# Optimization experiments

Hardware: AMD Instinct MI355X
Metric: run time of the kernel (lower is better)

Reference implementation:

```python
import jax, jax.numpy as jnp
import numpy as np

B, N, DIM_IN, DIM_INNER, DIM_OUT, WINDOW = 4, 4096, 1024, 1024, 1024, 128


def setup_inputs() -> dict:
    key = jax.random.key(0)
    k1, k2, k3, k4 = jax.random.split(key, 4)
    x = jax.random.normal(k1, (B, N, DIM_IN), dtype=jnp.float32)
    # to_qkv: Linear(dim_in, 3*dim_inner, bias=False); stored as [in, 3*inner] for x @ W
    w_qkv = jax.random.normal(k2, (DIM_IN, 3 * DIM_INNER), dtype=jnp.float32) / np.sqrt(DIM_IN)
    # to_out: Linear(dim_inner, dim_out) with bias
    w_out = jax.random.normal(k3, (DIM_INNER, DIM_OUT), dtype=jnp.float32) / np.sqrt(DIM_INNER)
    b_out = jax.random.normal(k4, (DIM_OUT,), dtype=jnp.float32) * 0.01
    return {"x": x, "w_qkv": w_qkv, "w_out": w_out, "b_out": b_out}


def reference(x, w_qkv, w_out, b_out):
    b, n, _ = x.shape
    w = WINDOW
    scale = DIM_INNER ** (-0.5)
    # n is a multiple of window, so pad_to_multiple is a no-op
    qkv = jnp.einsum('bnd,de->bne', x, w_qkv)
    q, k, v = jnp.split(qkv, 3, axis=-1)
    nw = n // w
    win = lambda t: t.reshape(b, nw, w, DIM_INNER)  # b (w n) d -> b w n d
    q, k, v = win(q), win(k), win(v)
    # pad one zero block at the front of the window axis
    kp = jnp.pad(k, ((0, 0), (1, 0), (0, 0), (0, 0)))
    # concat previous block + current block along token axis -> (b, nw, 2w, d)
    k2 = jnp.concatenate([kp[:, :-1], kp[:, 1:]], axis=2)
    # NOTE: faithful to source bug: the lambda references k (not t), so v is
    # overwritten with the concatenated k blocks as well.
    v2 = k2
    sim = jnp.einsum('bwid,bwjd->bwij', q, k2) * scale  # (b, nw, w, 2w)
    i, j = w, 2 * w
    mask = jnp.triu(jnp.ones((i, j), dtype=bool), j - i + 1)  # causal within lookback window
    mask_value = -jnp.finfo(sim.dtype).max
    sim = jnp.where(mask[None, None], mask_value, sim)
    attn = jax.nn.softmax(sim, axis=-1)
    out = jnp.einsum('bwij,bwjd->bwid', attn, v2)
    out = out.reshape(b, n, DIM_INNER)[:, :n]
    return jnp.einsum('bnd,de->bne', out, w_out) + b_out
```

## Files before the change

### kernel.cpp

```cpp
#include <hip/hip_runtime.h>
#include <float.h>


#define B_SZ 4
#define SEQ 4096
#define DIM 1024
#define WIN 128
#define NWIN 32
#define TW 256
#define NROWS (B_SZ * SEQ)
#define KPAD 4224

typedef float f32x4 __attribute__((ext_vector_type(4)));
typedef __bf16 bf16x8 __attribute__((ext_vector_type(8)));

__device__ __forceinline__ unsigned short f2b(float f) {
    unsigned int u = __float_as_uint(f);
    u += 0x7FFF + ((u >> 16) & 1);
    return (unsigned short)(u >> 16);
}

__device__ __forceinline__ void gld_lds16(const unsigned short* g, unsigned short* l) {
    __builtin_amdgcn_global_load_lds(
        (const __attribute__((address_space(1))) void*)g,
        (__attribute__((address_space(3))) void*)l, 16, 0, 0);
}

__device__ __forceinline__ bf16x8 lds_read_swz(const unsigned short* tb, int row, int kbyte) {
    int L = row * 128 + kbyte;
    L ^= ((L >> 9) & 1) << 5;
    return *(const bf16x8*)((const char*)tb + L);
}

#define BAR __builtin_amdgcn_s_barrier()
#define PRI1 __builtin_amdgcn_s_setprio(1)
#define PRI0 __builtin_amdgcn_s_setprio(0)
#define WAIT_LGKM0 do { asm volatile("s_waitcnt lgkmcnt(0)" ::: "memory"); \
                        __builtin_amdgcn_sched_barrier(0); } while (0)
#define WAIT_VM8   do { asm volatile("s_waitcnt vmcnt(8)" ::: "memory");  \
                        __builtin_amdgcn_sched_barrier(0); } while (0)
#define WAIT_VM0   do { asm volatile("s_waitcnt vmcnt(0)" ::: "memory");  \
                        __builtin_amdgcn_sched_barrier(0); } while (0)

#define LDAF(BUF, MH)                                                        \
    _Pragma("unroll") for (int m_ = 0; m_ < 4; ++m_)                         \
    _Pragma("unroll") for (int ks_ = 0; ks_ < 2; ++ks_)                      \
        afq[MH][m_][ks_] = lds_read_swz(bufA[BUF],                           \
            wr * 128 + (MH) * 64 + m_ * 16 + fr, ks_ * 64 + kby);

#define LDBF(BUF, NH)                                                        \
    _Pragma("unroll") for (int n_ = 0; n_ < 2; ++n_)                         \
    _Pragma("unroll") for (int ks_ = 0; ks_ < 2; ++ks_)                      \
        bfq[n_][ks_] = lds_read_swz(bufB[BUF],                               \
            wc * 64 + (NH) * 32 + n_ * 16 + fr, ks_ * 64 + kby);

#define MFQ(MH, NH)                                                          \
    _Pragma("unroll") for (int ks_ = 0; ks_ < 2; ++ks_)                      \
    _Pragma("unroll") for (int m_ = 0; m_ < 4; ++m_)                         \
    _Pragma("unroll") for (int n_ = 0; n_ < 2; ++n_)                         \
        acc[(MH) * 4 + m_][(NH) * 2 + n_] =                                  \
            __builtin_amdgcn_mfma_f32_16x16x32_bf16(afq[MH][m_][ks_],        \
                bfq[n_][ks_], acc[(MH) * 4 + m_][(NH) * 2 + n_], 0, 0, 0);

#define STG_A(BUF, HJ, K0) gld_lds16(A + soffA[HJ] + (K0), bufA[BUF] + ldst[HJ])
#define STG_B(BUF, HJ, K0) gld_lds16(Bt + soffB[HJ] + (K0), bufB[BUF] + ldst[HJ])

#define PHASES03(BUF, KST, ST)                                               \
    LDAF(BUF, 0); LDBF(BUF, 0);                                              \
    BAR; WAIT_LGKM0; PRI1; MFQ(0, 0); PRI0; BAR;                             \
    LDAF(BUF, 1);                                                            \
    BAR; WAIT_LGKM0; PRI1; MFQ(1, 0); PRI0; BAR;                             \
    LDBF(BUF, 1);                                                            \
    if (ST) { STG_A(BUF, 0, KST); STG_A(BUF, 1, KST);                        \
              STG_A(BUF, 2, KST); STG_A(BUF, 3, KST); }                      \
    BAR; WAIT_LGKM0; PRI1; MFQ(1, 1); PRI0; BAR;                             \
    if (ST) { STG_B(BUF, 0, KST); STG_B(BUF, 1, KST);                        \
              STG_B(BUF, 2, KST); STG_B(BUF, 3, KST); }                      \
    BAR; WAIT_LGKM0; PRI1; MFQ(0, 1); PRI0;

__device__ __forceinline__ void core256(
    const unsigned short* __restrict__ A, int lda,
    const unsigned short* __restrict__ Bt, int ldb, int K,
    unsigned short* lds, f32x4 (&acc)[8][4],
    int wid, int lane, int wr, int wc)
{
    unsigned short* bufA[2] = { lds, lds + 32768 };
    unsigned short* bufB[2] = { lds + 16384, lds + 49152 };

    const int kby = (lane >> 4) * 16;
    const int fr = lane & 15;

    int soffA[4], soffB[4], ldst[4];
#pragma unroll
    for (int hj = 0; hj < 4; ++hj) {
        const int half = hj >> 1, j = hj & 1;
        const int P = half * 16384 + wid * 2048 + j * 1024 + lane * 16;
        const int L = P ^ (((P >> 9) & 1) << 5);
        const int row = L >> 7, col = (L & 127) >> 1;
        soffA[hj] = row * lda + col;
        soffB[hj] = row * ldb + col;
        ldst[hj] = (half * 16384 + wid * 2048 + j * 1024) >> 1;
    }

    bf16x8 afq[2][4][2], bfq[2][2];
#pragma unroll
    for (int m = 0; m < 8; ++m)
#pragma unroll
        for (int n = 0; n < 4; ++n) acc[m][n] = (f32x4){0.f, 0.f, 0.f, 0.f};

#pragma unroll
    for (int hj = 0; hj < 4; ++hj) STG_A(0, hj, 0);
#pragma unroll
    for (int hj = 0; hj < 4; ++hj) STG_B(0, hj, 0);
#pragma unroll
    for (int hj = 0; hj < 4; ++hj) STG_A(1, hj, 64);
#pragma unroll
    for (int hj = 0; hj < 4; ++hj) STG_B(1, hj, 64);
    WAIT_VM8;
    BAR;

    const int NITER = K >> 7;
#pragma unroll 1
    for (int i = 0; i < NITER; ++i) {
        const bool st = (i + 1 < NITER);
        const int ka = (2 * i + 2) * 64;
        const int kb = (2 * i + 3) * 64;
        PHASES03(0, ka, st)
        if (st) { WAIT_VM8; } else { WAIT_VM0; }
        BAR;
        PHASES03(1, kb, st)
        if (st) { WAIT_VM8; }
        BAR;
    }
}

__device__ __forceinline__ void mfma_core(
    const unsigned short* __restrict__ A, int lda,
    const unsigned short* __restrict__ Bt, int ldb, int K,
    unsigned short* As, unsigned short* Bs, f32x4 (&acc)[4][4])
{
    const int tid = threadIdx.x;
    const int wv = tid >> 6, lane = tid & 63;
    const int wr = wv >> 1, wc = wv & 1;

#pragma unroll
    for (int m = 0; m < 4; ++m)
#pragma unroll
        for (int n = 0; n < 4; ++n) acc[m][n] = (f32x4){0.f, 0.f, 0.f, 0.f};

    for (int k0 = 0; k0 < K; k0 += 64) {
#pragma unroll
        for (int it = 0; it < 4; ++it) {
            int rbase = wv * 32 + it * 8;
            const unsigned short* g =
                A + (size_t)(rbase + (lane >> 3)) * lda + k0 + (lane & 7) * 8;
            gld_lds16(g, As + rbase * 64);
        }
#pragma unroll
        for (int it = 0; it < 4; ++it) {
            int rbase = wv * 32 + it * 8;
            const unsigned short* g =
                Bt + (size_t)(rbase + (lane >> 3)) * ldb + k0 + (lane & 7) * 8;
            gld_lds16(g, Bs + rbase * 64);
        }
        __syncthreads();

#pragma unroll
        for (int ks = 0; ks < 2; ++ks) {
            bf16x8 af[4], bfr[4];
            const int kof = ks * 32 + (lane >> 4) * 8;
#pragma unroll
            for (int m = 0; m < 4; ++m)
                af[m] = *(const bf16x8*)(As + (wr * 64 + m * 16 + (lane & 15)) * 64 + kof);
#pragma unroll
            for (int n = 0; n < 4; ++n)
                bfr[n] = *(const bf16x8*)(Bs + (wc * 64 + n * 16 + (lane & 15)) * 64 + kof);
#pragma unroll
            for (int m = 0; m < 4; ++m)
#pragma unroll
                for (int n = 0; n < 4; ++n)
                    acc[m][n] = __builtin_amdgcn_mfma_f32_16x16x32_bf16(
                        af[m], bfr[n], acc[m][n], 0, 0, 0);
        }
        __syncthreads();
    }
}

__global__ __launch_bounds__(256) void k_prep_x(const float* __restrict__ x,
                                                unsigned short* __restrict__ xb)
{
    int i = blockIdx.x * 256 + threadIdx.x;
    float4 a = *(const float4*)&x[(size_t)i * 8];
    float4 b = *(const float4*)&x[(size_t)i * 8 + 4];
    ushort4 lo, hi;
    lo.x = f2b(a.x); lo.y = f2b(a.y); lo.z = f2b(a.z); lo.w = f2b(a.w);
    hi.x = f2b(b.x); hi.y = f2b(b.y); hi.z = f2b(b.z); hi.w = f2b(b.w);
    *(ushort4*)&xb[(size_t)i * 8] = lo;
    *(ushort4*)&xb[(size_t)i * 8 + 4] = hi;
}

__global__ __launch_bounds__(256) void k_transpose(const float* __restrict__ src,
    int src_ld, int col0, int R, unsigned short* __restrict__ dst)
{
    __shared__ float T[32][33];
    const int r0 = blockIdx.y * 32, c0 = blockIdx.x * 32;
    const int cx = threadIdx.x & 31, ry = threadIdx.x >> 5;
#pragma unroll
    for (int i = 0; i < 4; ++i)
        T[ry + 8 * i][cx] = src[(size_t)(r0 + ry + 8 * i) * src_ld + col0 + c0 + cx];
    __syncthreads();
#pragma unroll
    for (int i = 0; i < 4; ++i)
        dst[(size_t)(c0 + ry + 8 * i) * R + r0 + cx] = f2b(T[cx][ry + 8 * i]);
}

__global__ __launch_bounds__(256) void k_zero_kpad(unsigned short* __restrict__ kbuf)
{
    int t = blockIdx.x * 256 + threadIdx.x;
    int b = t >> 14, r = t & 16383;
    float4 z = {0.f, 0.f, 0.f, 0.f};
    *(float4*)&kbuf[(size_t)b * KPAD * DIM + (size_t)r * 8] = z;
}

__global__ __launch_bounds__(256) void k_zero_ktpad(unsigned short* __restrict__ ktr)
{
    int t = blockIdx.x * 256 + threadIdx.x;
    int b = t >> 14, rem = t & 16383;
    int d = rem >> 4, s = rem & 15;
    float4 z = {0.f, 0.f, 0.f, 0.f};
    *(float4*)&ktr[((size_t)b * DIM + d) * KPAD + s * 8] = z;
}

__global__ __launch_bounds__(512, 2) void k_gemm_qk(
    const unsigned short* __restrict__ xb, const unsigned short* __restrict__ wqkvT,
    unsigned short* __restrict__ qbuf, unsigned short* __restrict__ kbuf,
    unsigned short* __restrict__ ktr)
{
    __shared__ unsigned short lds[65536];
    const int tid = threadIdx.x, wid = tid >> 6, lane = tid & 63;
    const int wr = wid >> 2, wc = wid & 3;
    const int wg = blockIdx.x;
    const int x = (wg & 7) * 64 + (wg >> 3);
    const int bm = (x & 63) * 256;
    const int bn = (x >> 6) * 256;

    f32x4 acc[8][4];
    core256(xb + (size_t)bm * DIM, DIM, wqkvT + (size_t)bn * DIM, DIM, DIM,
            lds, acc, wid, lane, wr, wc);

    const int fr = lane & 15;
#pragma unroll
    for (int m = 0; m < 8; ++m) {
        const int row0 = bm + wr * 128 + m * 16 + (lane >> 4) * 4;
#pragma unroll
        for (int n = 0; n < 4; ++n) {
            const int col = bn + wc * 64 + n * 16 + fr;
            if (col < DIM) {
#pragma unroll
                for (int r = 0; r < 4; ++r)
                    qbuf[(size_t)(row0 + r) * DIM + col] = f2b(acc[m][n][r]);
            } else {
                const int d = col - DIM;
                const int b = row0 >> 12, tok0 = row0 & 4095;
#pragma unroll
                for (int r = 0; r < 4; ++r)
                    kbuf[((size_t)b * KPAD + 128 + tok0 + r) * DIM + d] = f2b(acc[m][n][r]);
                ushort4 kt;
                kt.x = f2b(acc[m][n][0]); kt.y = f2b(acc[m][n][1]);
                kt.z = f2b(acc[m][n][2]); kt.w = f2b(acc[m][n][3]);
                *(ushort4*)&ktr[((size_t)b * DIM + d) * KPAD + 128 + tok0] = kt;
            }
        }
    }
}

__global__ __launch_bounds__(512, 2) void k_out(
    const unsigned short* __restrict__ aout, const unsigned short* __restrict__ woutT,
    const float* __restrict__ bias, float* __restrict__ out)
{
    __shared__ unsigned short lds[65536];
    const int tid = threadIdx.x, wid = tid >> 6, lane = tid & 63;
    const int wr = wid >> 2, wc = wid & 3;
    const int wg = blockIdx.x;
    const int x = (wg & 7) * 32 + (wg >> 3);
    const int bm = (x & 63) * 256;
    const int bn = (x >> 6) * 256;

    f32x4 acc[8][4];
    core256(aout + (size_t)bm * DIM, DIM, woutT + (size_t)bn * DIM, DIM, DIM,
            lds, acc, wid, lane, wr, wc);

    const int fr = lane & 15;
#pragma unroll
    for (int m = 0; m < 8; ++m) {
        const int row0 = bm + wr * 128 + m * 16 + (lane >> 4) * 4;
#pragma unroll
        for (int n = 0; n < 4; ++n) {
            const int col = bn + wc * 64 + n * 16 + fr;
            const float bb = bias[col];
#pragma unroll
            for (int r = 0; r < 4; ++r)
                out[(size_t)(row0 + r) * DIM + col] = acc[m][n][r] + bb;
        }
    }
}

__global__ __launch_bounds__(256) void k_sim(
    const unsigned short* __restrict__ qbuf, const unsigned short* __restrict__ kbuf,
    float* __restrict__ sim)
{
    __shared__ unsigned short As[128 * 64], Bs[128 * 64];
    f32x4 acc[4][4];
    const int win = blockIdx.y, ct = blockIdx.x;
    const int b = win >> 5, w = win & 31;
    const unsigned short* Ap = qbuf + ((size_t)b * SEQ + w * WIN) * DIM;
    const unsigned short* Bp = kbuf + ((size_t)b * KPAD + w * WIN + ct * 128) * DIM;
    mfma_core(Ap, DIM, Bp, DIM, DIM, As, Bs, acc);

    const int tid = threadIdx.x, wv = tid >> 6, lane = tid & 63;
    const int wr = wv >> 1, wc = wv & 1;
    const float scale = 0.03125f;
#pragma unroll
    for (int m = 0; m < 4; ++m) {
        const int qi0 = wr * 64 + m * 16 + (lane >> 4) * 4;
#pragma unroll
        for (int n = 0; n < 4; ++n) {
            const int jc = ct * 128 + wc * 64 + n * 16 + (lane & 15);
#pragma unroll
            for (int r = 0; r < 4; ++r) {
                const int qi = qi0 + r;
                float v = (jc > qi + WIN) ? -FLT_MAX : acc[m][n][r] * scale;
                sim[((size_t)win * WIN + qi) * TW + jc] = v;
            }
        }
    }
}

__global__ __launch_bounds__(256) void k_softmax(const float* __restrict__ sim,
                                                 unsigned short* __restrict__ attnb)
{
    const int row = blockIdx.x * 4 + (threadIdx.x >> 6);
    const int lane = threadIdx.x & 63;
    const float* p = sim + (size_t)row * TW;
    float4 v = *(const float4*)&p[lane * 4];
    float m = fmaxf(fmaxf(v.x, v.y), fmaxf(v.z, v.w));
#pragma unroll
    for (int off = 32; off; off >>= 1) m = fmaxf(m, __shfl_xor(m, off));
    float e0 = expf(v.x - m), e1 = expf(v.y - m);
    float e2 = expf(v.z - m), e3 = expf(v.w - m);
    float s = e0 + e1 + e2 + e3;
#pragma unroll
    for (int off = 32; off; off >>= 1) s += __shfl_xor(s, off);
    float inv = 1.f / s;
    ushort4 o;
    o.x = f2b(e0 * inv); o.y = f2b(e1 * inv); o.z = f2b(e2 * inv); o.w = f2b(e3 * inv);
    *(ushort4*)&attnb[(size_t)row * TW + lane * 4] = o;
}

__global__ __launch_bounds__(256) void k_pv(
    const unsigned short* __restrict__ attnb, const unsigned short* __restrict__ ktr,
    unsigned short* __restrict__ aout)
{
    __shared__ unsigned short As[128 * 64], Bs[128 * 64];
    f32x4 acc[4][4];
    const int win = blockIdx.y, ct = blockIdx.x;
    const int b = win >> 5, w = win & 31;
    const unsigned short* Ap = attnb + (size_t)win * WIN * TW;
    const unsigned short* Bp = ktr + ((size_t)b * DIM + ct * 128) * KPAD + w * WIN;
    mfma_core(Ap, TW, Bp, KPAD, TW, As, Bs, acc);

    const int tid = threadIdx.x, wv = tid >> 6, lane = tid & 63;
    const int wr = wv >> 1, wc = wv & 1;
#pragma unroll
    for (int m = 0; m < 4; ++m) {
        const int row0 = wr * 64 + m * 16 + (lane >> 4) * 4;
#pragma unroll
        for (int n = 0; n < 4; ++n) {
            const int col = ct * 128 + wc * 64 + n * 16 + (lane & 15);
#pragma unroll
            for (int r = 0; r < 4; ++r)
                aout[((size_t)b * SEQ + w * WIN + row0 + r) * DIM + col] =
                    f2b(acc[m][n][r]);
        }
    }
}

extern "C" void kernel_launch(void* const* d_in, const int* in_sizes, int n_in,
                              void* d_out, int out_size, void* d_ws, size_t ws_size,
                              hipStream_t stream)
{
    const float* x     = (const float*)d_in[0];
    const float* w_qkv = (const float*)d_in[1];
    const float* w_out = (const float*)d_in[2];
    const float* b_out = (const float*)d_in[3];
    float* out = (float*)d_out;

    char* p = (char*)d_ws;
    unsigned short* xb    = (unsigned short*)p; p += (size_t)NROWS * DIM * 2;
    unsigned short* wqkvT = (unsigned short*)p; p += (size_t)2 * DIM * DIM * 2;
    unsigned short* woutT = (unsigned short*)p; p += (size_t)DIM * DIM * 2;
    unsigned short* qbuf  = (unsigned short*)p; p += (size_t)NROWS * DIM * 2;
    unsigned short* kbuf  = (unsigned short*)p; p += (size_t)B_SZ * KPAD * DIM * 2;
    unsigned short* ktr   = (unsigned short*)p; p += (size_t)B_SZ * DIM * KPAD * 2;
    float*          simb  = (float*)p;          p += (size_t)NROWS * TW * 4;
    unsigned short* attnb = (unsigned short*)p; p += (size_t)NROWS * TW * 2;
    unsigned short* aout  = (unsigned short*)p; p += (size_t)NROWS * DIM * 2;

    k_prep_x<<<NROWS * DIM / 8 / 256, 256, 0, stream>>>(x, xb);
    k_transpose<<<dim3(2 * DIM / 32, DIM / 32), 256, 0, stream>>>(w_qkv, 3 * DIM, 0, DIM, wqkvT);
    k_transpose<<<dim3(DIM / 32, DIM / 32), 256, 0, stream>>>(w_out, DIM, 0, DIM, woutT);
    k_zero_kpad<<<256, 256, 0, stream>>>(kbuf);
    k_zero_ktpad<<<256, 256, 0, stream>>>(ktr);

    k_gemm_qk<<<512, 512, 0, stream>>>(xb, wqkvT, qbuf, kbuf, ktr);
    k_sim<<<dim3(2, B_SZ * NWIN), 256, 0, stream>>>(qbuf, kbuf, simb);
    k_softmax<<<NROWS / 4, 256, 0, stream>>>(simb, attnb);
    k_pv<<<dim3(DIM / 128, B_SZ * NWIN), 256, 0, stream>>>(attnb, ktr, aout);
    k_out<<<256, 512, 0, stream>>>(aout, woutT, b_out, out);
}
```

Baseline: 380.7 us.

## Interleave global-to-LDS staging at half-tile granularity across GEMM phases

Restructures the double-buffered GEMM main loop so global-to-LDS loads are issued in half-tile pieces spread across all eight MFMA phases, rather than whole A and B tiles in two phases per buffer. The second buffer's last B half is deferred into the next iteration, and vmcnt waits become finer (4/6 instead of 8). The goal is smoother memory traffic and better overlap of loads with MFMA work. It adds scheduling complexity and a risk of LDS hazards if the wait counts do not match the outstanding loads.

```diff
diff --git a/kernel.cpp b/kernel.cpp
--- a/kernel.cpp
+++ b/kernel.cpp
@@ -35,12 +35,10 @@
 #define BAR __builtin_amdgcn_s_barrier()
 #define PRI1 __builtin_amdgcn_s_setprio(1)
 #define PRI0 __builtin_amdgcn_s_setprio(0)
-#define WAIT_LGKM0 do { asm volatile("s_waitcnt lgkmcnt(0)" ::: "memory"); \
-                        __builtin_amdgcn_sched_barrier(0); } while (0)
-#define WAIT_VM8   do { asm volatile("s_waitcnt vmcnt(8)" ::: "memory");  \
-                        __builtin_amdgcn_sched_barrier(0); } while (0)
-#define WAIT_VM0   do { asm volatile("s_waitcnt vmcnt(0)" ::: "memory");  \
-                        __builtin_amdgcn_sched_barrier(0); } while (0)
+#define LGKM0 do { asm volatile("s_waitcnt lgkmcnt(0)" ::: "memory"); \
+                   __builtin_amdgcn_sched_barrier(0); } while (0)
+#define VMW(N) do { asm volatile("s_waitcnt vmcnt(" #N ")" ::: "memory"); \
+                    __builtin_amdgcn_sched_barrier(0); } while (0)
 
 #define LDAF(BUF, MH)                                                        \
     _Pragma("unroll") for (int m_ = 0; m_ < 4; ++m_)                         \
@@ -62,21 +60,12 @@
             __builtin_amdgcn_mfma_f32_16x16x32_bf16(afq[MH][m_][ks_],        \
                 bfq[n_][ks_], acc[(MH) * 4 + m_][(NH) * 2 + n_], 0, 0, 0);
 
-#define STG_A(BUF, HJ, K0) gld_lds16(A + soffA[HJ] + (K0), bufA[BUF] + ldst[HJ])
-#define STG_B(BUF, HJ, K0) gld_lds16(Bt + soffB[HJ] + (K0), bufB[BUF] + ldst[HJ])
-
-#define PHASES03(BUF, KST, ST)                                               \
-    LDAF(BUF, 0); LDBF(BUF, 0);                                              \
-    BAR; WAIT_LGKM0; PRI1; MFQ(0, 0); PRI0; BAR;                             \
-    LDAF(BUF, 1);                                                            \
-    BAR; WAIT_LGKM0; PRI1; MFQ(1, 0); PRI0; BAR;                             \
-    LDBF(BUF, 1);                                                            \
-    if (ST) { STG_A(BUF, 0, KST); STG_A(BUF, 1, KST);                        \
-              STG_A(BUF, 2, KST); STG_A(BUF, 3, KST); }                      \
-    BAR; WAIT_LGKM0; PRI1; MFQ(1, 1); PRI0; BAR;                             \
-    if (ST) { STG_B(BUF, 0, KST); STG_B(BUF, 1, KST);                        \
-              STG_B(BUF, 2, KST); STG_B(BUF, 3, KST); }                      \
-    BAR; WAIT_LGKM0; PRI1; MFQ(0, 1); PRI0;
+#define STG_HA(BUF, HALF, K0)                                                \
+    { gld_lds16(A + soffA[(HALF) * 2 + 0] + (K0), bufA[BUF] + ldst[(HALF) * 2 + 0]); \
+      gld_lds16(A + soffA[(HALF) * 2 + 1] + (K0), bufA[BUF] + ldst[(HALF) * 2 + 1]); }
+#define STG_HB(BUF, HALF, K0)                                                \
+    { gld_lds16(Bt + soffB[(HALF) * 2 + 0] + (K0), bufB[BUF] + ldst[(HALF) * 2 + 0]); \
+      gld_lds16(Bt + soffB[(HALF) * 2 + 1] + (K0), bufB[BUF] + ldst[(HALF) * 2 + 1]); }
 
 __device__ __forceinline__ void core256(
     const unsigned short* __restrict__ A, int lda,
@@ -108,29 +97,40 @@
 #pragma unroll
         for (int n = 0; n < 4; ++n) acc[m][n] = (f32x4){0.f, 0.f, 0.f, 0.f};
 
-#pragma unroll
-    for (int hj = 0; hj < 4; ++hj) STG_A(0, hj, 0);
-#pragma unroll
-    for (int hj = 0; hj < 4; ++hj) STG_B(0, hj, 0);
-#pragma unroll
-    for (int hj = 0; hj < 4; ++hj) STG_A(1, hj, 64);
-#pragma unroll
-    for (int hj = 0; hj < 4; ++hj) STG_B(1, hj, 64);
-    WAIT_VM8;
+    STG_HA(0, 0, 0); STG_HA(0, 1, 0); STG_HB(0, 0, 0); STG_HB(0, 1, 0);
+    STG_HA(1, 0, 64); STG_HA(1, 1, 64); STG_HB(1, 0, 64);
+    VMW(6);
     BAR;
 
     const int NITER = K >> 7;
 #pragma unroll 1
     for (int i = 0; i < NITER; ++i) {
         const bool st = (i + 1 < NITER);
-        const int ka = (2 * i + 2) * 64;
-        const int kb = (2 * i + 3) * 64;
-        PHASES03(0, ka, st)
-        if (st) { WAIT_VM8; } else { WAIT_VM0; }
-        BAR;
-        PHASES03(1, kb, st)
-        if (st) { WAIT_VM8; }
-        BAR;
+        const int ku1 = (2 * i + 1) * 64;
+        const int ku2 = (2 * i + 2) * 64;
+        const int ku3 = (2 * i + 3) * 64;
+
+        LDAF(0, 0); LDBF(0, 0);
+        STG_HB(1, 1, ku1);
+        BAR; LGKM0; PRI1; MFQ(0, 0); PRI0; BAR;
+        LDAF(0, 1);
+        BAR; LGKM0; PRI1; MFQ(1, 0); PRI0; BAR;
+        LDBF(0, 1);
+        if (st) STG_HA(0, 0, ku2);
+        BAR; LGKM0; PRI1; MFQ(1, 1); PRI0; BAR;
+        if (st) { STG_HA(0, 1, ku2); VMW(4); } else { VMW(0); }
+        BAR; PRI1; MFQ(0, 1); PRI0; BAR;
+        LDAF(1, 0); LDBF(1, 0);
+        if (st) STG_HB(0, 0, ku2);
+        BAR; LGKM0; PRI1; MFQ(0, 0); PRI0; BAR;
+        LDAF(1, 1);
+        if (st) STG_HB(0, 1, ku2);
+        BAR; LGKM0; PRI1; MFQ(1, 0); PRI0; BAR;
+        LDBF(1, 1);
+        if (st) STG_HA(1, 0, ku3);
+        BAR; LGKM0; PRI1; MFQ(1, 1); PRI0; BAR;
+        if (st) { STG_HA(1, 1, ku3); STG_HB(1, 0, ku3); VMW(6); } else { VMW(0); }
+        BAR; PRI1; MFQ(0, 1); PRI0; BAR;
     }
 }
 
```

New measurement: 366.1 us. -3.8%, faster.
